# Kernel tuning notes

Hardware: AMD Instinct MI355X
Metric: run time of the kernel (lower is better)

## Reference

```python
import jax, jax.numpy as jnp
import numpy as np

DIM = 512
HEADS = 8
HEAD_DIM = DIM // HEADS
EPS = 1e-5

def _ln(x, g, b):
    m = jnp.mean(x, axis=-1, keepdims=True)
    v = jnp.mean((x - m) ** 2, axis=-1, keepdims=True)
    return (x - m) * jax.lax.rsqrt(v + EPS) * g + b

def setup_inputs() -> dict:
    key = jax.random.key(0)
    ks = jax.random.split(key, 12)
    s = 0.02
    d, dff = DIM, 4 * DIM
    inp = {
        'x': jax.random.normal(ks[0], (8, 4096, d), jnp.float32),
        'Wq': jax.random.normal(ks[1], (d, d), jnp.float32) * s,
        'bq': jnp.zeros((d,), jnp.float32),
        'Wk': jax.random.normal(ks[2], (d, d), jnp.float32) * s,
        'bk': jnp.zeros((d,), jnp.float32),
        'Wv': jax.random.normal(ks[3], (d, d), jnp.float32) * s,
        'bv': jnp.zeros((d,), jnp.float32),
        'Wo': jax.random.normal(ks[4], (d, d), jnp.float32) * s,
        'bo': jnp.zeros((d,), jnp.float32),
        'g1': jnp.ones((d,), jnp.float32),
        'b1': jnp.zeros((d,), jnp.float32),
        'g2': jnp.ones((d,), jnp.float32),
        'b2': jnp.zeros((d,), jnp.float32),
        'Wf1': jax.random.normal(ks[5], (d, dff), jnp.float32) * s,
        'bf1': jnp.zeros((dff,), jnp.float32),
        'Wf2': jax.random.normal(ks[6], (dff, d), jnp.float32) * s,
        'bf2': jnp.zeros((d,), jnp.float32),
    }
    return inp

def _linear_attn(x, Wq, bq, Wk, bk, Wv, bv, Wo, bo):
    b, n, d = x.shape
    def split(t):
        return t.reshape(b, n, HEADS, HEAD_DIM).transpose(0, 2, 1, 3)  # bhnd
    q = split(x @ Wq + bq)
    k = split(x @ Wk + bk)
    v = split(x @ Wv + bv)
    q = jax.nn.elu(q) + 1.0
    k = jax.nn.elu(k) + 1.0
    kv = jnp.einsum('bhnd,bhnf->bhdf', k, v)
    out = jnp.einsum('bhnd,bhdf->bhnf', q, kv)
    out = out.transpose(0, 2, 1, 3).reshape(b, n, d)
    return out @ Wo + bo

def reference(x, Wq, bq, Wk, bk, Wv, bv, Wo, bo, g1, b1, g2, b2, Wf1, bf1, Wf2, bf2):
    # series decomposition: AvgPool1d(k=3, stride=1, pad=1, count_include_pad=True)
    xp = jnp.pad(x, ((0, 0), (1, 1), (0, 0)))
    trend = (xp[:, :-2] + xp[:, 1:-1] + xp[:, 2:]) / 3.0
    seasonal = x - trend
    seasonal = seasonal + _linear_attn(_ln(seasonal, g1, b1), Wq, bq, Wk, bk, Wv, bv, Wo, bo)
    h = _ln(seasonal, g2, b2)
    h = jax.nn.gelu(h @ Wf1 + bf1, approximate=False) @ Wf2 + bf2
    seasonal = seasonal + h
    return seasonal + trend
```

## Files before the change

### kernel.cpp

```cpp
#include <hip/hip_runtime.h>
#include <math.h>

typedef __bf16 bf16;
typedef __attribute__((ext_vector_type(8))) __bf16 bf16x8;
typedef __attribute__((ext_vector_type(4))) float floatx4;

#define DIM 512
#define DFF 2048
#define SEQ 4096
#define ROWS 32768

#define GLOBAL_AS(p) ((const __attribute__((address_space(1))) void*)(p))
#define LDS_AS(p)    ((__attribute__((address_space(3))) void*)(p))

__global__ __launch_bounds__(256) void prep_w_kernel(const float* __restrict__ W,
                                                     bf16* __restrict__ Wt, int K, int N)
{
    int idx = blockIdx.x * 256 + threadIdx.x;
    if (idx >= K * N) return;
    int k = idx % K;
    int n = idx / K;
    Wt[idx] = (bf16)W[(size_t)k * N + n];
}

__global__ __launch_bounds__(256) void prep_w3_kernel(const float* __restrict__ Wq,
                                                      const float* __restrict__ Wk,
                                                      const float* __restrict__ Wv,
                                                      bf16* __restrict__ Wt)
{
    int idx = blockIdx.x * 256 + threadIdx.x;
    int which = idx >> 18;
    int r = idx & 262143;
    int k = r & 511;
    int n = r >> 9;
    const float* W = (which == 0) ? Wq : (which == 1 ? Wk : Wv);
    Wt[idx] = (bf16)W[(size_t)k * 512 + n];
}

__global__ __launch_bounds__(256) void pack_bias_kernel(const float* __restrict__ bq,
                                                        const float* __restrict__ bk,
                                                        const float* __restrict__ bv,
                                                        float* __restrict__ out)
{
    int i = blockIdx.x * 256 + threadIdx.x;
    if (i >= 1536) return;
    out[i] = (i < 512) ? bq[i] : (i < 1024 ? bk[i - 512] : bv[i - 1024]);
}

__device__ inline float wave_red(float v)
{
#pragma unroll
    for (int off = 32; off; off >>= 1) v += __shfl_xor(v, off, 64);
    return v;
}

__global__ __launch_bounds__(256) void decomp_ln_kernel(const float* __restrict__ x,
                                                        const float* __restrict__ g,
                                                        const float* __restrict__ be,
                                                        float* __restrict__ S,
                                                        bf16* __restrict__ XN)
{
    int wave = threadIdx.x >> 6, lane = threadIdx.x & 63;
    int r = blockIdx.x * 4 + wave;
    int n = r & (SEQ - 1);
    const float4* xr = (const float4*)(x + (size_t)r * DIM);
    float4 z = make_float4(0.f, 0.f, 0.f, 0.f);
    float s[8];
#pragma unroll
    for (int i = 0; i < 2; ++i) {
        int c4 = lane * 2 + i;
        float4 v0 = xr[c4];
        float4 vm = (n > 0)       ? xr[c4 - DIM / 4] : z;
        float4 vp = (n < SEQ - 1) ? xr[c4 + DIM / 4] : z;
        s[i * 4 + 0] = v0.x - (vm.x + v0.x + vp.x) * (1.f / 3.f);
        s[i * 4 + 1] = v0.y - (vm.y + v0.y + vp.y) * (1.f / 3.f);
        s[i * 4 + 2] = v0.z - (vm.z + v0.z + vp.z) * (1.f / 3.f);
        s[i * 4 + 3] = v0.w - (vm.w + v0.w + vp.w) * (1.f / 3.f);
    }
    float4* Sr = (float4*)(S + (size_t)r * DIM);
    Sr[lane * 2]     = make_float4(s[0], s[1], s[2], s[3]);
    Sr[lane * 2 + 1] = make_float4(s[4], s[5], s[6], s[7]);

    float sum = 0.f;
#pragma unroll
    for (int j = 0; j < 8; ++j) sum += s[j];
    sum = wave_red(sum);
    float mean = sum * (1.f / DIM);
    float vs = 0.f;
#pragma unroll
    for (int j = 0; j < 8; ++j) { float d = s[j] - mean; vs += d * d; }
    vs = wave_red(vs);
    float rstd = rsqrtf(vs * (1.f / DIM) + 1e-5f);

    int c = lane * 8;
    float4 g0 = ((const float4*)(g + c))[0],  g1v = ((const float4*)(g + c))[1];
    float4 b0 = ((const float4*)(be + c))[0], b1v = ((const float4*)(be + c))[1];
    bf16x8 o;
    o[0] = (bf16)((s[0] - mean) * rstd * g0.x + b0.x);
    o[1] = (bf16)((s[1] - mean) * rstd * g0.y + b0.y);
    o[2] = (bf16)((s[2] - mean) * rstd * g0.z + b0.z);
    o[3] = (bf16)((s[3] - mean) * rstd * g0.w + b0.w);
    o[4] = (bf16)((s[4] - mean) * rstd * g1v.x + b1v.x);
    o[5] = (bf16)((s[5] - mean) * rstd * g1v.y + b1v.y);
    o[6] = (bf16)((s[6] - mean) * rstd * g1v.z + b1v.z);
    o[7] = (bf16)((s[7] - mean) * rstd * g1v.w + b1v.w);
    *(bf16x8*)(XN + (size_t)r * DIM + c) = o;
}

__global__ __launch_bounds__(256) void ln_kernel(const float* __restrict__ X,
                                                 const float* __restrict__ g,
                                                 const float* __restrict__ be,
                                                 bf16* __restrict__ XN)
{
    int wave = threadIdx.x >> 6, lane = threadIdx.x & 63;
    int r = blockIdx.x * 4 + wave;
    const float4* xr = (const float4*)(X + (size_t)r * DIM);
    float4 a0 = xr[lane * 2], a1 = xr[lane * 2 + 1];
    float s[8] = {a0.x, a0.y, a0.z, a0.w, a1.x, a1.y, a1.z, a1.w};
    float sum = 0.f;
#pragma unroll
    for (int j = 0; j < 8; ++j) sum += s[j];
    sum = wave_red(sum);
    float mean = sum * (1.f / DIM);
    float vs = 0.f;
#pragma unroll
    for (int j = 0; j < 8; ++j) { float d = s[j] - mean; vs += d * d; }
    vs = wave_red(vs);
    float rstd = rsqrtf(vs * (1.f / DIM) + 1e-5f);
    int c = lane * 8;
    float4 g0 = ((const float4*)(g + c))[0],  g1v = ((const float4*)(g + c))[1];
    float4 b0 = ((const float4*)(be + c))[0], b1v = ((const float4*)(be + c))[1];
    bf16x8 o;
    o[0] = (bf16)((s[0] - mean) * rstd * g0.x + b0.x);
    o[1] = (bf16)((s[1] - mean) * rstd * g0.y + b0.y);
    o[2] = (bf16)((s[2] - mean) * rstd * g0.z + b0.z);
    o[3] = (bf16)((s[3] - mean) * rstd * g0.w + b0.w);
    o[4] = (bf16)((s[4] - mean) * rstd * g1v.x + b1v.x);
    o[5] = (bf16)((s[5] - mean) * rstd * g1v.y + b1v.y);
    o[6] = (bf16)((s[6] - mean) * rstd * g1v.z + b1v.z);
    o[7] = (bf16)((s[7] - mean) * rstd * g1v.w + b1v.w);
    *(bf16x8*)(XN + (size_t)r * DIM + c) = o;
}

enum { M_QKV = 0, M_ATTN = 1, M_FFN1 = 2, M_FFN2 = 3 };

template <int MODE>
__global__ __launch_bounds__(256) void gemm_bt_kernel(const bf16* __restrict__ A, int lda,
                                                      const bf16* __restrict__ Bt,
                                                      const float* __restrict__ bias,
                                                      float* S, const float* __restrict__ X,
                                                      void* Cout, int ldc,
                                                      int N, int K, int rows_per_batch,
                                                      int m_off)
{
    __shared__ __align__(16) bf16 lA[2][128 * 32];
    __shared__ __align__(16) bf16 lB[2][128 * 32];
    int tid = threadIdx.x;

    int nwg = gridDim.x * gridDim.y;
    int orig = blockIdx.y * gridDim.x + blockIdx.x;
    int wg = (orig & 7) * (nwg >> 3) + (orig >> 3);
    int m0 = (wg / gridDim.x) * 128;
    int n0 = (wg % gridDim.x) * 128;

    const bf16* Abase = A + (size_t)m0 * lda;
    const bf16* Bbase = Bt + (size_t)n0 * K;
    if (rows_per_batch) Bbase += (size_t)(m0 / rows_per_batch) * (size_t)N * K;

    int lane = tid & 63;
    int wave = tid >> 6;
    int wm = (wave >> 1) * 64;
    int wn = (wave & 1) * 64;
    int lm = lane & 15;
    int quad = lane >> 4;
    int i0w = tid & 192;

    floatx4 acc[4][4];
#pragma unroll
    for (int i = 0; i < 4; ++i)
#pragma unroll
        for (int j = 0; j < 4; ++j) acc[i][j] = (floatx4){0.f, 0.f, 0.f, 0.f};

    auto stage = [&](int buf, int k0) {
#pragma unroll
        for (int it = 0; it < 2; ++it) {
            int ib = it * 256 + i0w;
            int i  = ib + lane;
            int row = i >> 2;
            int col = (i & 3) * 8;
            __builtin_amdgcn_global_load_lds(GLOBAL_AS(Abase + (size_t)row * lda + k0 + col),
                                             LDS_AS(&lA[buf][ib * 8]), 16, 0, 0);
            __builtin_amdgcn_global_load_lds(GLOBAL_AS(Bbase + (size_t)row * K + k0 + col),
                                             LDS_AS(&lB[buf][ib * 8]), 16, 0, 0);
        }
    };

    stage(0, 0);
    int cur = 0;
    for (int k0 = 0; k0 < K; k0 += 32) {
        __syncthreads();
        if (k0 + 32 < K) stage(cur ^ 1, k0 + 32);
        bf16x8 af[4], bfv[4];
#pragma unroll
        for (int i = 0; i < 4; ++i)
            af[i] = *(const bf16x8*)&lA[cur][(wm + i * 16 + lm) * 32 + quad * 8];
#pragma unroll
        for (int j = 0; j < 4; ++j)
            bfv[j] = *(const bf16x8*)&lB[cur][(wn + j * 16 + lm) * 32 + quad * 8];
#pragma unroll
        for (int i = 0; i < 4; ++i)
#pragma unroll
            for (int j = 0; j < 4; ++j)
                acc[i][j] = __builtin_amdgcn_mfma_f32_16x16x32_bf16(af[i], bfv[j], acc[i][j], 0, 0, 0);
        cur ^= 1;
    }

#pragma unroll
    for (int i = 0; i < 4; ++i) {
        int gm_base = m0 + wm + i * 16 + quad * 4;
#pragma unroll
        for (int j = 0; j < 4; ++j) {
            int gn = n0 + wn + j * 16 + lm;
            float bia = bias[gn];
#pragma unroll
            for (int e = 0; e < 4; ++e) {
                int gm = gm_base + e;
                float val = acc[i][j][e] + bia;
                if constexpr (MODE == M_QKV) {
                    if (gn < 1024) val = (val > 0.f) ? val + 1.f : __expf(val);
                    ((bf16*)Cout)[(size_t)gm * ldc + gn] = (bf16)val;
                } else if constexpr (MODE == M_ATTN) {
                    S[(size_t)gm * DIM + gn] += val;
                } else if constexpr (MODE == M_FFN1) {
                    val = 0.5f * val * (1.f + erff(val * 0.70710678118654752f));
                    ((bf16*)Cout)[(size_t)gm * ldc + gn] = (bf16)val;
                } else {
                    int gmg = m_off + gm;
                    int nn = gmg & (SEQ - 1);
                    size_t o = (size_t)gmg * DIM + gn;
                    float xc = X[o];
                    float xm = (nn > 0)       ? X[o - DIM] : 0.f;
                    float xp = (nn < SEQ - 1) ? X[o + DIM] : 0.f;
                    float* op = (float*)Cout;
                    op[o] = val + op[o] + (xm + xc + xp) * (1.f / 3.f);
                }
            }
        }
    }
}

__global__ __launch_bounds__(256) void kv_mfma_kernel(const bf16* __restrict__ QKV,
                                                      float* __restrict__ KV)
{
    int kc = blockIdx.x, h = blockIdx.y, b = blockIdx.z;
    __shared__ __align__(16) bf16 lbuf[2][2 * 128 * 64];
    int tid = threadIdx.x;
    int lane = tid & 63, wave = tid >> 6;
    int lm = lane & 15, quad = lane >> 4;

    floatx4 acc[4][4];
#pragma unroll
    for (int i = 0; i < 4; ++i)
#pragma unroll
        for (int j = 0; j < 4; ++j) acc[i][j] = (floatx4){0.f, 0.f, 0.f, 0.f};

    const bf16* kb = QKV + (size_t)b * SEQ * 1536 + 512 + (size_t)h * 64;
    const bf16* vb = kb + 512;
    int drow = lane >> 3;
    int d0 = (lane & 7) * 8;

    auto stage = [&](int buf, int it) {
        int n0 = kc * 1024 + it * 128;
#pragma unroll
        for (int q = 0; q < 4; ++q) {
            int nbase = wave * 32 + q * 8;
            int ldsoff = wave * 2048 + q * 512;
            __builtin_amdgcn_global_load_lds(GLOBAL_AS(kb + (size_t)(n0 + nbase + drow) * 1536 + d0),
                                             LDS_AS(&lbuf[buf][ldsoff]), 16, 0, 0);
            __builtin_amdgcn_global_load_lds(GLOBAL_AS(vb + (size_t)(n0 + nbase + drow) * 1536 + d0),
                                             LDS_AS(&lbuf[buf][8192 + ldsoff]), 16, 0, 0);
        }
    };

    stage(0, 0);
    int cur = 0;
    for (int it = 0; it < 8; ++it) {
        __syncthreads();
        if (it < 7) stage(cur ^ 1, it + 1);
        const bf16* lk = lbuf[cur];
        const bf16* lv = lbuf[cur] + 8192;

        int nw = wave * 32 + quad * 8;
        bf16x8 af[4], bfv[4];
#pragma unroll
        for (int i = 0; i < 4; ++i) {
            int dd = i * 16 + lm;
#pragma unroll
            for (int j = 0; j < 8; ++j) af[i][j] = lk[(nw + j) * 64 + dd];
#pragma unroll
            for (int j = 0; j < 8; ++j) bfv[i][j] = lv[(nw + j) * 64 + dd];
        }
#pragma unroll
        for (int i = 0; i < 4; ++i)
#pragma unroll
            for (int j = 0; j < 4; ++j)
                acc[i][j] = __builtin_amdgcn_mfma_f32_16x16x32_bf16(af[i], bfv[j], acc[i][j], 0, 0, 0);
        cur ^= 1;
    }

    __syncthreads();
    float* red = (float*)lbuf;
    if (wave < 2) {
#pragma unroll
        for (int i = 0; i < 4; ++i)
#pragma unroll
            for (int j = 0; j < 4; ++j)
#pragma unroll
                for (int e = 0; e < 4; ++e)
                    red[wave * 4096 + (i * 16 + quad * 4 + e) * 64 + j * 16 + lm] = acc[i][j][e];
    }
    __syncthreads();
    if (wave >= 2) {
#pragma unroll
        for (int i = 0; i < 4; ++i)
#pragma unroll
            for (int j = 0; j < 4; ++j)
#pragma unroll
                for (int e = 0; e < 4; ++e)
                    red[(wave - 2) * 4096 + (i * 16 + quad * 4 + e) * 64 + j * 16 + lm] += acc[i][j][e];
    }
    __syncthreads();
    float* dst = KV + ((size_t)kc * 64 + b * 8 + h) * 4096;
#pragma unroll
    for (int p = 0; p < 4; ++p) {
        int e4 = (tid + p * 256) * 4;
        float4 a = *(const float4*)&red[e4];
        float4 c4 = *(const float4*)&red[4096 + e4];
        a.x += c4.x; a.y += c4.y; a.z += c4.z; a.w += c4.w;
        *(float4*)&dst[e4] = a;
    }
}

__global__ __launch_bounds__(256) void kvw_kernel(const float* __restrict__ KV,
                                                  const float* __restrict__ Wo,
                                                  bf16* __restrict__ KVWT)
{
    int jc = blockIdx.x & 7, bh = blockIdx.x >> 3;
    int h = bh & 7, b = bh >> 3;
    __shared__ float skvT[64 * 68];
    int tid = threadIdx.x;
    const float* src = KV + (size_t)bh * 4096;
#pragma unroll
    for (int p = 0; p < 16; ++p) {
        int e = tid + p * 256;
        float s = src[e] + src[e + 262144] + src[e + 524288] + src[e + 786432];
        skvT[(e & 63) * 68 + (e >> 6)] = s;
    }
    __syncthreads();

    int j = tid & 63, dq = tid >> 6;
    int j0 = jc * 64;
    floatx4 acc4[4];
#pragma unroll
    for (int c = 0; c < 4; ++c) acc4[c] = (floatx4){0.f, 0.f, 0.f, 0.f};
    const float* wop = Wo + (size_t)h * 64 * 512 + j0 + j;
#pragma unroll 8
    for (int f = 0; f < 64; ++f) {
        float w = wop[(size_t)f * 512];
        const float* sp = &skvT[f * 68 + dq * 16];
#pragma unroll
        for (int c = 0; c < 4; ++c) {
            floatx4 s = *(const floatx4*)(sp + c * 4);
            acc4[c] += s * w;
        }
    }
    bf16* dst = KVWT + (size_t)b * 262144 + (size_t)(j0 + j) * 512 + h * 64 + dq * 16;
    bf16x8 o0, o1;
#pragma unroll
    for (int t = 0; t < 8; ++t) { o0[t] = (bf16)acc4[t >> 2][t & 3]; o1[t] = (bf16)acc4[2 + (t >> 2)][t & 3]; }
    *(bf16x8*)dst = o0;
    *(bf16x8*)(dst + 8) = o1;
}

extern "C" void kernel_launch(void* const* d_in, const int* in_sizes, int n_in,
                              void* d_out, int out_size, void* d_ws, size_t ws_size,
                              hipStream_t stream)
{
    const float* x   = (const float*)d_in[0];
    const float* Wq  = (const float*)d_in[1];
    const float* bq  = (const float*)d_in[2];
    const float* Wk  = (const float*)d_in[3];
    const float* bk  = (const float*)d_in[4];
    const float* Wv  = (const float*)d_in[5];
    const float* bv  = (const float*)d_in[6];
    const float* Wo  = (const float*)d_in[7];
    const float* bo  = (const float*)d_in[8];
    const float* g1  = (const float*)d_in[9];
    const float* b1  = (const float*)d_in[10];
    const float* g2  = (const float*)d_in[11];
    const float* b2  = (const float*)d_in[12];
    const float* Wf1 = (const float*)d_in[13];
    const float* bf1 = (const float*)d_in[14];
    const float* Wf2 = (const float*)d_in[15];
    const float* bf2 = (const float*)d_in[16];
    float* out = (float*)d_out;
    (void)in_sizes; (void)n_in; (void)out_size;

    char* ws = (char*)d_ws;
    size_t off = 0;
    auto alloc = [&](size_t bytes) -> char* {
        char* p = ws + off;
        off += (bytes + 255) & ~(size_t)255;
        return p;
    };
    bf16*  WqkvT = (bf16*)alloc((size_t)1536 * 512 * 2);
    float* bias3 = (float*)alloc(1536 * 4);
    bf16*  Wf1T  = (bf16*)alloc((size_t)2048 * 512 * 2);
    bf16*  Wf2T  = (bf16*)alloc((size_t)512 * 2048 * 2);
    size_t post_xn_off = 0;
    bf16*  XN    = (bf16*)alloc((size_t)ROWS * DIM * 2);
    post_xn_off = off;
    float* KV    = (float*)alloc((size_t)4 * 64 * 4096 * 4);
    bf16*  KVWT  = (bf16*)alloc((size_t)8 * 512 * 512 * 2);
    bf16*  QKV   = (bf16*)alloc((size_t)ROWS * 1536 * 2);

    size_t h1_bytes  = (size_t)ROWS * DFF * 2;
    bool   merged    = ws_size >= post_xn_off + h1_bytes;
    bf16*  H1full    = (bf16*)(ws + post_xn_off);
    bf16*  H1chunk   = QKV;

    prep_w3_kernel<<<3072, 256, 0, stream>>>(Wq, Wk, Wv, WqkvT);
    prep_w_kernel<<<4096, 256, 0, stream>>>(Wf1, Wf1T, 512, 2048);
    prep_w_kernel<<<4096, 256, 0, stream>>>(Wf2, Wf2T, 2048, 512);
    pack_bias_kernel<<<6, 256, 0, stream>>>(bq, bk, bv, bias3);

    decomp_ln_kernel<<<8192, 256, 0, stream>>>(x, g1, b1, out, XN);

    gemm_bt_kernel<M_QKV><<<dim3(12, 256), 256, 0, stream>>>(
        XN, 512, WqkvT, bias3, nullptr, nullptr, QKV, 1536, 1536, 512, 0, 0);

    kv_mfma_kernel<<<dim3(4, 8, 8), 256, 0, stream>>>(QKV, KV);

    kvw_kernel<<<512, 256, 0, stream>>>(KV, Wo, KVWT);

    gemm_bt_kernel<M_ATTN><<<dim3(4, 256), 256, 0, stream>>>(
        QKV, 1536, KVWT, bo, out, nullptr, nullptr, 0, 512, 512, 4096, 0);

    ln_kernel<<<8192, 256, 0, stream>>>(out, g2, b2, XN);

    if (merged) {
        gemm_bt_kernel<M_FFN1><<<dim3(16, 256), 256, 0, stream>>>(
            XN, 512, Wf1T, bf1, nullptr, nullptr, H1full, 2048, 2048, 512, 0, 0);
        gemm_bt_kernel<M_FFN2><<<dim3(4, 256), 256, 0, stream>>>(
            H1full, 2048, Wf2T, bf2, nullptr, x, out, 512, 512, 2048, 0, 0);
    } else {
        for (int c = 0; c < 2; ++c) {
            gemm_bt_kernel<M_FFN1><<<dim3(16, 128), 256, 0, stream>>>(
                XN + (size_t)c * 16384 * 512, 512, Wf1T, bf1, nullptr, nullptr,
                H1chunk, 2048, 2048, 512, 0, 0);
            gemm_bt_kernel<M_FFN2><<<dim3(4, 128), 256, 0, stream>>>(
                H1chunk, 2048, Wf2T, bf2, nullptr, x, out, 512, 512, 2048, 0, c * 16384);
        }
    }
}
```

Baseline: 678.4 us.

## Triple-buffer GEMM and KV staging with explicit vmcnt waits and XOR-swizzled LDS

Both the GEMM kernel and the KV MFMA kernel move from double to triple-buffered LDS staging, so each tile is prefetched two steps ahead. Explicit s_waitcnt vmcnt counts and raw barriers replace __syncthreads, so only the oldest outstanding loads must land before each step. The GEMM kernel also XOR-swizzles the k-chunk column by row to reduce LDS bank conflicts on the fragment reads. This raises LDS use per block, which may cut occupancy, and correctness depends on the hand-counted vmcnt values matching the number of async loads issued.

```diff
diff --git a/kernel.cpp b/kernel.cpp
--- a/kernel.cpp
+++ b/kernel.cpp
@@ -153,8 +153,8 @@
                                                       int N, int K, int rows_per_batch,
                                                       int m_off)
 {
-    __shared__ __align__(16) bf16 lA[2][128 * 32];
-    __shared__ __align__(16) bf16 lB[2][128 * 32];
+    __shared__ __align__(16) bf16 lA[3][128 * 32];
+    __shared__ __align__(16) bf16 lB[3][128 * 32];
     int tid = threadIdx.x;
 
     int nwg = gridDim.x * gridDim.y;
@@ -187,7 +187,7 @@
             int ib = it * 256 + i0w;
             int i  = ib + lane;
             int row = i >> 2;
-            int col = (i & 3) * 8;
+            int col = ((i & 3) ^ (row & 3)) * 8;
             __builtin_amdgcn_global_load_lds(GLOBAL_AS(Abase + (size_t)row * lda + k0 + col),
                                              LDS_AS(&lA[buf][ib * 8]), 16, 0, 0);
             __builtin_amdgcn_global_load_lds(GLOBAL_AS(Bbase + (size_t)row * K + k0 + col),
@@ -196,23 +196,41 @@
     };
 
     stage(0, 0);
+    stage(1, 32);
+    asm volatile("s_waitcnt vmcnt(4)" ::: "memory");
+    __builtin_amdgcn_s_barrier();
+
+    int nsteps = K >> 5;
     int cur = 0;
-    for (int k0 = 0; k0 < K; k0 += 32) {
-        __syncthreads();
-        if (k0 + 32 < K) stage(cur ^ 1, k0 + 32);
+    for (int s = 0; s < nsteps; ++s) {
+        int kpre = (s + 2) << 5;
+        bool issued = kpre < K;
+        if (issued) {
+            int nxt = cur + 2; if (nxt >= 3) nxt -= 3;
+            stage(nxt, kpre);
+        }
+
         bf16x8 af[4], bfv[4];
 #pragma unroll
-        for (int i = 0; i < 4; ++i)
-            af[i] = *(const bf16x8*)&lA[cur][(wm + i * 16 + lm) * 32 + quad * 8];
-#pragma unroll
-        for (int j = 0; j < 4; ++j)
-            bfv[j] = *(const bf16x8*)&lB[cur][(wn + j * 16 + lm) * 32 + quad * 8];
+        for (int i = 0; i < 4; ++i) {
+            int ra = wm + i * 16 + lm;
+            af[i] = *(const bf16x8*)&lA[cur][ra * 32 + (quad ^ (ra & 3)) * 8];
+        }
+#pragma unroll
+        for (int j = 0; j < 4; ++j) {
+            int rb = wn + j * 16 + lm;
+            bfv[j] = *(const bf16x8*)&lB[cur][rb * 32 + (quad ^ (rb & 3)) * 8];
+        }
 #pragma unroll
         for (int i = 0; i < 4; ++i)
 #pragma unroll
             for (int j = 0; j < 4; ++j)
                 acc[i][j] = __builtin_amdgcn_mfma_f32_16x16x32_bf16(af[i], bfv[j], acc[i][j], 0, 0, 0);
-        cur ^= 1;
+
+        if (issued) asm volatile("s_waitcnt vmcnt(4)" ::: "memory");
+        else        asm volatile("s_waitcnt vmcnt(0)" ::: "memory");
+        __builtin_amdgcn_s_barrier();
+        cur = (cur == 2) ? 0 : cur + 1;
     }
 
 #pragma unroll
@@ -253,7 +271,7 @@
                                                       float* __restrict__ KV)
 {
     int kc = blockIdx.x, h = blockIdx.y, b = blockIdx.z;
-    __shared__ __align__(16) bf16 lbuf[2][2 * 128 * 64];
+    __shared__ __align__(16) bf16 lbuf[3][2 * 128 * 64];
     int tid = threadIdx.x;
     int lane = tid & 63, wave = tid >> 6;
     int lm = lane & 15, quad = lane >> 4;
@@ -283,10 +301,17 @@
     };
 
     stage(0, 0);
+    stage(1, 1);
+    asm volatile("s_waitcnt vmcnt(8)" ::: "memory");
+    __builtin_amdgcn_s_barrier();
+
     int cur = 0;
     for (int it = 0; it < 8; ++it) {
-        __syncthreads();
-        if (it < 7) stage(cur ^ 1, it + 1);
+        bool issued = (it + 2) < 8;
+        if (issued) {
+            int nxt = cur + 2; if (nxt >= 3) nxt -= 3;
+            stage(nxt, it + 2);
+        }
         const bf16* lk = lbuf[cur];
         const bf16* lv = lbuf[cur] + 8192;
 
@@ -305,7 +330,11 @@
 #pragma unroll
             for (int j = 0; j < 4; ++j)
                 acc[i][j] = __builtin_amdgcn_mfma_f32_16x16x32_bf16(af[i], bfv[j], acc[i][j], 0, 0, 0);
-        cur ^= 1;
+
+        if (issued) asm volatile("s_waitcnt vmcnt(8)" ::: "memory");
+        else        asm volatile("s_waitcnt vmcnt(0)" ::: "memory");
+        __builtin_amdgcn_s_barrier();
+        cur = (cur == 2) ? 0 : cur + 1;
     }
 
     __syncthreads();
```

Result: no change. 682.0 us (+0.5%).
